# Performance work log

Hardware: AMD Instinct MI355X
Metric: run time of the kernel (lower is better)

The kernel has to match this reference:

```python
import jax, jax.numpy as jnp
import numpy as np
from jax import lax

B, D_MODEL, H, W = 8, 384, 64, 64
D_INNER, D_STATE, D_CONV, DT_RANK = 768, 16, 4, 24
C3, MLP_H = 3 * D_MODEL, 4 * D_MODEL
EPS = 1e-5


def setup_inputs():
    key = jax.random.key(0)
    ks = jax.random.split(key, 16)
    r = lambda i, shape, s=0.02: jax.random.normal(ks[i], shape, jnp.float32) * s
    return {
        'x': jax.random.normal(ks[0], (B, D_MODEL, H, W), jnp.float32),
        'ln1_g': jnp.ones((D_MODEL,), jnp.float32), 'ln1_b': jnp.zeros((D_MODEL,), jnp.float32),
        'in_w': r(1, (2 * D_INNER, D_MODEL)),
        'conv_w': r(2, (D_INNER, 1, D_CONV), 0.2), 'conv_b': jnp.zeros((D_INNER,), jnp.float32),
        'xproj_w': r(3, (DT_RANK + 2 * D_STATE, D_INNER)),
        'dtproj_w': r(4, (D_INNER, DT_RANK), 0.1),
        'dtproj_b': jnp.full((D_INNER,), jnp.log(jnp.expm1(0.01)).item(), jnp.float32),
        'A_log': jnp.log(jnp.broadcast_to(jnp.arange(1, D_STATE + 1, dtype=jnp.float32), (D_INNER, D_STATE))),
        'Dskip': jnp.ones((D_INNER,), jnp.float32),
        'out_w': r(5, (D_MODEL, D_INNER)),
        'dw_w': r(6, (C3, 1, 3, 3), 0.1),
        'bn_g': jnp.ones((C3,), jnp.float32), 'bn_b': jnp.zeros((C3,), jnp.float32),
        'bn_mean': jnp.zeros((C3,), jnp.float32), 'bn_var': jnp.ones((C3,), jnp.float32),
        'pw_w': r(7, (C3, C3)),
        'fus_w': r(8, (D_MODEL, D_MODEL)), 'fus_b': jnp.zeros((D_MODEL,), jnp.float32),
        'ln2_g': jnp.ones((D_MODEL,), jnp.float32), 'ln2_b': jnp.zeros((D_MODEL,), jnp.float32),
        'mlp_w1': r(9, (MLP_H, D_MODEL)), 'mlp_b1': jnp.zeros((MLP_H,), jnp.float32),
        'mlp_w2': r(10, (D_MODEL, MLP_H)), 'mlp_b2': jnp.zeros((D_MODEL,), jnp.float32),
    }


def _ln(x, g, b):
    m = x.mean(-1, keepdims=True)
    v = ((x - m) ** 2).mean(-1, keepdims=True)
    return (x - m) / jnp.sqrt(v + EPS) * g + b


def _dwt(x):
    x01 = x[:, :, 0::2, :] / 2
    x02 = x[:, :, 1::2, :] / 2
    x1, x3 = x01[:, :, :, 0::2], x01[:, :, :, 1::2]
    x2, x4 = x02[:, :, :, 0::2], x02[:, :, :, 1::2]
    ll = x1 + x2 + x3 + x4
    hl = -x1 - x2 + x3 + x4
    lh = -x1 + x2 - x3 + x4
    hh = x1 - x2 - x3 + x4
    return ll, jnp.concatenate([hl, lh, hh], axis=1)


def _idwt(ll, high):
    b, c, h, w = ll.shape
    hl, lh, hh = jnp.split(high, 3, axis=1)
    h_ll, h_hl, h_lh, h_hh = ll / 2, hl / 2, lh / 2, hh / 2
    y1 = h_ll - h_hl - h_lh + h_hh  # (even row, even col)
    y2 = h_ll - h_hl + h_lh - h_hh  # (odd row, even col)
    y3 = h_ll + h_hl - h_lh - h_hh  # (even row, odd col)
    y4 = h_ll + h_hl + h_lh + h_hh  # (odd row, odd col)
    row_e = jnp.stack([y1, y3], axis=-1).reshape(b, c, h, 2 * w)
    row_o = jnp.stack([y2, y4], axis=-1).reshape(b, c, h, 2 * w)
    return jnp.stack([row_e, row_o], axis=-2).reshape(b, c, 2 * h, 2 * w)


def _mamba(x, in_w, conv_w, conv_b, xproj_w, dtproj_w, dtproj_b, A_log, Dskip, out_w):
    # x: [B, L, d_model]
    bb = x.shape[0]
    xz = x @ in_w.T  # [B,L,2*d_inner]
    xi, z = jnp.split(xz, 2, axis=-1)
    xc = jnp.swapaxes(xi, 1, 2)  # [B,d_inner,L]
    xc = lax.conv_general_dilated(xc, conv_w, (1,), [(D_CONV - 1, 0)],
                                  feature_group_count=D_INNER,
                                  dimension_numbers=('NCH', 'OIH', 'NCH')) + conv_b[None, :, None]
    u = jax.nn.silu(jnp.swapaxes(xc, 1, 2))  # [B,L,d_inner]
    dbl = u @ xproj_w.T
    dtr = dbl[..., :DT_RANK]
    Bm = dbl[..., DT_RANK:DT_RANK + D_STATE]
    Cm = dbl[..., DT_RANK + D_STATE:]
    dt = jax.nn.softplus(dtr @ dtproj_w.T + dtproj_b)  # [B,L,d_inner]
    A = -jnp.exp(A_log)  # [d_inner,d_state]

    def step(h, t):
        dt_t, B_t, C_t, u_t = t
        dA = jnp.exp(dt_t[:, :, None] * A)
        h = dA * h + (dt_t * u_t)[:, :, None] * B_t[:, None, :]
        return h, jnp.sum(h * C_t[:, None, :], axis=-1)

    h0 = jnp.zeros((bb, D_INNER, D_STATE), x.dtype)
    xs = (jnp.swapaxes(dt, 0, 1), jnp.swapaxes(Bm, 0, 1), jnp.swapaxes(Cm, 0, 1), jnp.swapaxes(u, 0, 1))
    _, ys = lax.scan(step, h0, xs)
    y = jnp.swapaxes(ys, 0, 1) + u * Dskip
    y = y * jax.nn.silu(z)
    return y @ out_w.T


def reference(x, ln1_g, ln1_b, in_w, conv_w, conv_b, xproj_w, dtproj_w, dtproj_b,
              A_log, Dskip, out_w, dw_w, bn_g, bn_b, bn_mean, bn_var, pw_w,
              fus_w, fus_b, ln2_g, ln2_b, mlp_w1, mlp_b1, mlp_w2, mlp_b2):
    shortcut = x
    x_ll, x_high = _dwt(x)
    b, c, hh, ww = x_ll.shape
    # LL branch: LN -> Mamba -> residual
    x_ll_in = _ln(jnp.transpose(x_ll, (0, 2, 3, 1)), ln1_g, ln1_b)
    y = _mamba(x_ll_in.reshape(b, hh * ww, c), in_w, conv_w, conv_b, xproj_w,
               dtproj_w, dtproj_b, A_log, Dskip, out_w)
    x_ll_out = x_ll + jnp.transpose(y.reshape(b, hh, ww, c), (0, 3, 1, 2))
    # High-freq branch: depthwise3x3 -> BN(eval) -> SiLU -> 1x1 -> residual
    hd = lax.conv_general_dilated(x_high, dw_w, (1, 1), [(1, 1), (1, 1)],
                                  feature_group_count=C3,
                                  dimension_numbers=('NCHW', 'OIHW', 'NCHW'))
    hd = (hd - bn_mean[None, :, None, None]) / jnp.sqrt(bn_var + EPS)[None, :, None, None] \
         * bn_g[None, :, None, None] + bn_b[None, :, None, None]
    hd = jax.nn.silu(hd)
    x_high_out = x_high + jnp.einsum('bchw,oc->bohw', hd, pw_w)
    # Reconstruct + fusion 1x1 conv + residual
    recon = _idwt(x_ll_out, x_high_out)
    recon = jnp.einsum('bchw,oc->bohw', recon, fus_w) + fus_b[None, :, None, None]
    x2 = shortcut + recon
    # LN + MLP + residual
    xn = _ln(jnp.transpose(x2, (0, 2, 3, 1)), ln2_g, ln2_b)
    m = jax.nn.gelu(xn @ mlp_w1.T + mlp_b1, approximate=False) @ mlp_w2.T + mlp_b2
    return x2 + jnp.transpose(m, (0, 3, 1, 2))
```

## Files before the change

### kernel.cpp

```cpp
#include <hip/hip_runtime.h>
#include <hip/hip_bf16.h>
#include <math.h>

typedef __hip_bfloat16 bf16;
typedef __attribute__((ext_vector_type(8))) short bf16x8;
typedef __attribute__((ext_vector_type(4))) float f32x4;
typedef unsigned short u16;

#define LN_EPS 1e-5f

__device__ inline u16 f2b(float v) {
    __hip_bfloat16 h = __float2bfloat16(v);
    return *reinterpret_cast<u16*>(&h);
}

__device__ inline float b2f_lo(unsigned int w) { return __uint_as_float(w << 16); }
__device__ inline float b2f_hi(unsigned int w) { return __uint_as_float(w & 0xFFFF0000u); }

__device__ inline void gload_lds16(const void* g, void* l) {
    __builtin_amdgcn_global_load_lds(
        (const __attribute__((address_space(1))) void*)(uintptr_t)g,
        (__attribute__((address_space(3))) void*)(uintptr_t)(unsigned int)(uintptr_t)l,
        16, 0, 0);
}
__device__ inline void gload_lds4(const void* g, void* l) {
    __builtin_amdgcn_global_load_lds(
        (const __attribute__((address_space(1))) void*)(uintptr_t)g,
        (__attribute__((address_space(3))) void*)(uintptr_t)(unsigned int)(uintptr_t)l,
        4, 0, 0);
}

__global__ __launch_bounds__(256) void sentinel_kernel(float* __restrict__ out, int n) {
    int i = blockIdx.x * 256 + threadIdx.x;
    if (i < n) out[i] = 123.0f;
}

__global__ __launch_bounds__(256) void reduce12_kernel(const float* __restrict__ P,
                                                       float* __restrict__ out, int n4) {
    int i = blockIdx.x * 256 + threadIdx.x;
    if (i >= n4) return;
    const float4* p4 = (const float4*)P;
    float4 s = p4[i];
#pragma unroll
    for (int z = 1; z < 12; z++) {
        float4 v = p4[(size_t)z * n4 + i];
        s.x += v.x; s.y += v.y; s.z += v.z; s.w += v.w;
    }
    ((float4*)out)[i] = s;
}

__global__ void detect_kernel(const unsigned int* __restrict__ g, int* __restrict__ flag) {
    *flag = (*g == 0x3F803F80u) ? 1 : 0;
}

struct Jobs {
    const void* src[25];
    int prefix[26];
};
__global__ __launch_bounds__(256) void convert_kernel(Jobs J, u16* __restrict__ dst16,
                                                      float* __restrict__ dst32,
                                                      const int* __restrict__ flag) {
    int i = blockIdx.x * 256 + threadIdx.x;
    int total = J.prefix[25];
    if (i >= total) return;
    int f = *flag;
    int lo = 0;
    while (J.prefix[lo + 1] <= i) lo++;
    int off = i - J.prefix[lo];
    float v = f ? (float)((const bf16*)J.src[lo])[off] : ((const float*)J.src[lo])[off];
    if (lo < 6) dst16[i] = f2b(v);
    else        dst32[i - J.prefix[6]] = v;
}

__global__ __launch_bounds__(256) void dwt_kernel(const void* __restrict__ xv,
                                                  float* __restrict__ xll,
                                                  float* __restrict__ xhigh,
                                                  const int* __restrict__ flag) {
    __shared__ float tile[32][133];
    int blk = blockIdx.x;
    int cc = blk % 12;
    int t2 = blk / 12;
    int i  = t2 % 32;
    int b  = t2 / 32;
    int t  = threadIdx.x;
    int c_l = t >> 3;
    int sub = t & 7;
    size_t rowbase = ((size_t)(b * 384 + cc * 32 + c_l)) * 4096 + (size_t)i * 128;
    if (*flag) {
        const u16* xp = (const u16*)xv + rowbase;
#pragma unroll
        for (int k = 0; k < 2; k++) {
            int e0 = (sub + k * 8) * 8;
            uint4 v = *(const uint4*)(xp + e0);
            tile[c_l][e0 + 0] = b2f_lo(v.x); tile[c_l][e0 + 1] = b2f_hi(v.x);
            tile[c_l][e0 + 2] = b2f_lo(v.y); tile[c_l][e0 + 3] = b2f_hi(v.y);
            tile[c_l][e0 + 4] = b2f_lo(v.z); tile[c_l][e0 + 5] = b2f_hi(v.z);
            tile[c_l][e0 + 6] = b2f_lo(v.w); tile[c_l][e0 + 7] = b2f_hi(v.w);
        }
    } else {
        const float* xp = (const float*)xv + rowbase;
#pragma unroll
        for (int k = 0; k < 4; k++) {
            int f0 = (sub + k * 8) * 4;
            float4 v = *(const float4*)(xp + f0);
            tile[c_l][f0 + 0] = v.x; tile[c_l][f0 + 1] = v.y;
            tile[c_l][f0 + 2] = v.z; tile[c_l][f0 + 3] = v.w;
        }
    }
    __syncthreads();
    int c_out = t & 31;
    int jg = t >> 5;
    int cg = cc * 32 + c_out;
#pragma unroll
    for (int jj = 0; jj < 4; jj++) {
        int j = jg * 4 + jj;
        float A = tile[c_out][2 * j];
        float B = tile[c_out][2 * j + 1];
        float C = tile[c_out][64 + 2 * j];
        float D = tile[c_out][64 + 2 * j + 1];
        float ll = 0.5f * (A + B + C + D);
        float hl = 0.5f * (B + D - A - C);
        float lh = 0.5f * (C + D - A - B);
        float hh = 0.5f * (A + D - B - C);
        int pm = b * 1024 + i * 32 + j;
        xll[(size_t)pm * 384 + cg] = ll;
        size_t hb = (size_t)pm * 1152;
        xhigh[hb + cg] = hl;
        xhigh[hb + 384 + cg] = lh;
        xhigh[hb + 768 + cg] = hh;
    }
}

template <bool OBF>
__global__ __launch_bounds__(128) void ln_kernel(const float* __restrict__ in,
                                                 void* __restrict__ outv,
                                                 const float* __restrict__ g,
                                                 const float* __restrict__ b) {
    const int C = 384;
    int row = blockIdx.x;
    int t = threadIdx.x;
    const float* rp = in + (size_t)row * C;
    float v0 = rp[t], v1 = rp[t + 128], v2 = rp[t + 256];
    __shared__ float red[128];
    red[t] = v0 + v1 + v2;
    __syncthreads();
    for (int off = 64; off > 0; off >>= 1) {
        if (t < off) red[t] += red[t + off];
        __syncthreads();
    }
    float mean = red[0] * (1.f / 384.f);
    __syncthreads();
    float d0 = v0 - mean, d1 = v1 - mean, d2 = v2 - mean;
    red[t] = d0 * d0 + d1 * d1 + d2 * d2;
    __syncthreads();
    for (int off = 64; off > 0; off >>= 1) {
        if (t < off) red[t] += red[t + off];
        __syncthreads();
    }
    float inv = rsqrtf(red[0] * (1.f / 384.f) + LN_EPS);
    float o0 = d0 * inv * g[t]       + b[t];
    float o1 = d1 * inv * g[t + 128] + b[t + 128];
    float o2 = d2 * inv * g[t + 256] + b[t + 256];
    if constexpr (OBF) {
        u16* op = (u16*)outv + (size_t)row * C;
        op[t] = f2b(o0); op[t + 128] = f2b(o1); op[t + 256] = f2b(o2);
    } else {
        float* op = (float*)outv + (size_t)row * C;
        op[t] = o0; op[t + 128] = o1; op[t + 256] = o2;
    }
}

#define EP_NONE 0
#define EP_SOFTPLUS_BIAS 1
#define EP_ADD 2
#define EP_FUS 3
#define EP_GELU_BIAS 4
#define EP_FINAL 5

template <int EPIL, bool CBF>
__global__ __launch_bounds__(256) void gemm_mfma(const u16* __restrict__ A, int lda,
                                                 const u16* __restrict__ W,
                                                 void* __restrict__ Cp, int ldc,
                                                 int M, int N, int K,
                                                 const float* __restrict__ addsrc,
                                                 const float* __restrict__ bias,
                                                 const void* __restrict__ xres,
                                                 void* __restrict__ obf,
                                                 int m_off,
                                                 const int* __restrict__ flag) {
    __shared__ u16 Als[2][128][32];
    __shared__ u16 Bls[2][128][32];
    const int t = threadIdx.x;
    const int wave = t >> 6, lane = t & 63;
    const int quad = lane >> 4, r16 = lane & 15;
    const int wm = (wave >> 1) * 64, wn = (wave & 1) * 64;
    const int mb = blockIdx.x * 128, nb = blockIdx.y * 128;
    f32x4 acc[4][4] = {};

    const int srow = wave * 32 + (lane >> 2);
    const int scol = (lane & 3) * 8;
    const u16* Ag0 = A + (size_t)(mb + srow) * lda + scol;
    const u16* Ag1 = A + (size_t)(mb + srow + 16) * lda + scol;
    const u16* Wg0 = W + (size_t)(nb + srow) * (size_t)K + scol;
    const u16* Wg1 = W + (size_t)(nb + srow + 16) * (size_t)K + scol;

    gload_lds16(Ag0, &Als[0][wave * 32][0]);
    gload_lds16(Ag1, &Als[0][wave * 32 + 16][0]);
    gload_lds16(Wg0, &Bls[0][wave * 32][0]);
    gload_lds16(Wg1, &Bls[0][wave * 32 + 16][0]);
    __syncthreads();

    int cur = 0;
    for (int k0 = 0; k0 < K; k0 += 32) {
        int nxt = cur ^ 1;
        if (k0 + 32 < K) {
            gload_lds16(Ag0 + k0 + 32, &Als[nxt][wave * 32][0]);
            gload_lds16(Ag1 + k0 + 32, &Als[nxt][wave * 32 + 16][0]);
            gload_lds16(Wg0 + k0 + 32, &Bls[nxt][wave * 32][0]);
            gload_lds16(Wg1 + k0 + 32, &Bls[nxt][wave * 32 + 16][0]);
        }
        bf16x8 af[4], bfv[4];
#pragma unroll
        for (int i = 0; i < 4; i++) af[i] = *(const bf16x8*)&Als[cur][wm + i * 16 + r16][quad * 8];
#pragma unroll
        for (int j = 0; j < 4; j++) bfv[j] = *(const bf16x8*)&Bls[cur][wn + j * 16 + r16][quad * 8];
#pragma unroll
        for (int i = 0; i < 4; i++)
#pragma unroll
            for (int j = 0; j < 4; j++)
                acc[i][j] = __builtin_amdgcn_mfma_f32_16x16x32_bf16(af[i], bfv[j], acc[i][j], 0, 0, 0);
        __syncthreads();
        cur = nxt;
    }

    int f = 0;
    if constexpr (EPIL == EP_FUS || EPIL == EP_FINAL) f = *flag;
#pragma unroll
    for (int i = 0; i < 4; i++) {
#pragma unroll
        for (int j = 0; j < 4; j++) {
#pragma unroll
            for (int rg = 0; rg < 4; rg++) {
                int m = mb + wm + i * 16 + quad * 4 + rg;
                int n = nb + wn + j * 16 + r16;
                float v = acc[i][j][rg];
                if constexpr (EPIL == EP_NONE) {
                    if constexpr (CBF) ((u16*)Cp)[(size_t)m * ldc + n] = f2b(v);
                    else               ((float*)Cp)[(size_t)m * ldc + n] = v;
                } else if constexpr (EPIL == EP_ADD) {
                    ((float*)Cp)[(size_t)m * ldc + n] = addsrc[(size_t)m * ldc + n] + v;
                } else if constexpr (EPIL == EP_FUS) {
                    v += bias[n];
                    int bb = m >> 12, pix = m & 4095;
                    size_t xi = ((size_t)(bb * 384 + n) << 12) + pix;
                    v += f ? (float)((const bf16*)xres)[xi] : ((const float*)xres)[xi];
                    ((float*)Cp)[(size_t)m * ldc + n] = v;
                } else if constexpr (EPIL == EP_GELU_BIAS) {
                    v += bias[n];
                    v = 0.5f * v * (1.f + erff(v * 0.70710678118654752f));
                    if constexpr (CBF) ((u16*)Cp)[(size_t)m * ldc + n] = f2b(v);
                    else               ((float*)Cp)[(size_t)m * ldc + n] = v;
                } else if constexpr (EPIL == EP_FINAL) {
                    v += bias[n];
                    int gm = m_off + m;
                    v += addsrc[(size_t)gm * 384 + n];
                    int bb = gm >> 12, pix = gm & 4095;
                    size_t oi = ((size_t)(bb * 384 + n) << 12) + pix;
                    if (f) ((bf16*)obf)[oi] = __float2bfloat16(v);
                    else   ((float*)obf)[oi] = v;
                }
            }
        }
    }
}

template <int EPIL, bool SPLITK>
__global__ __launch_bounds__(256) void gemm_nt(const float* __restrict__ A, int lda,
                                               const float* __restrict__ W,
                                               float* __restrict__ C, int ldc,
                                               int M, int N, int K,
                                               const float* __restrict__ bias,
                                               int kc) {
    __shared__ __align__(16) float As[16][68];
    __shared__ __align__(16) float Bs[16][68];
    int t = threadIdx.x;
    int mb = blockIdx.y * 64;
    int nb = blockIdx.x * 64;
    int kb = SPLITK ? blockIdx.z * kc : 0;
    int ke = SPLITK ? kb + kc : K;
    int tm = t & 15, tn = t >> 4;
    float* Cout = C;
    if constexpr (SPLITK) Cout = C + (size_t)blockIdx.z * (size_t)M * ldc;
    float acc[4][4] = {};
    for (int k0 = kb; k0 < ke; k0 += 16) {
#pragma unroll
        for (int i = 0; i < 4; i++) {
            int idx = t + i * 256;
            int r = idx >> 4, c = idx & 15;
            float v = 0.f;
            if (k0 + c < K) v = A[(size_t)(mb + r) * lda + k0 + c];
            As[c][r] = v;
        }
#pragma unroll
        for (int i = 0; i < 4; i++) {
            int idx = t + i * 256;
            int r = idx >> 4, c = idx & 15;
            float v = 0.f;
            if ((nb + r) < N && (k0 + c) < K) v = W[(size_t)(nb + r) * K + k0 + c];
            Bs[c][r] = v;
        }
        __syncthreads();
#pragma unroll
        for (int kk = 0; kk < 16; kk++) {
            float4 av = *(const float4*)&As[kk][tm * 4];
            float4 bv = *(const float4*)&Bs[kk][tn * 4];
            float a4[4] = {av.x, av.y, av.z, av.w};
            float b4[4] = {bv.x, bv.y, bv.z, bv.w};
#pragma unroll
            for (int i = 0; i < 4; i++)
#pragma unroll
                for (int j = 0; j < 4; j++) acc[i][j] += a4[i] * b4[j];
        }
        __syncthreads();
    }
#pragma unroll
    for (int i = 0; i < 4; i++) {
        int m = mb + tm * 4 + i;
        if (m >= M) continue;
#pragma unroll
        for (int j = 0; j < 4; j++) {
            int n = nb + tn * 4 + j;
            if (n >= N) continue;
            float v = acc[i][j];
            if constexpr (SPLITK) {
                Cout[(size_t)m * ldc + n] = v;
            } else if constexpr (EPIL == EP_NONE) {
                C[(size_t)m * ldc + n] = v;
            } else if constexpr (EPIL == EP_SOFTPLUS_BIAS) {
                v += bias[n];
                v = (v > 20.f) ? v : log1pf(expf(v));
                C[(size_t)m * ldc + n] = v;
            }
        }
    }
}

__global__ __launch_bounds__(256) void conv1d_silu_kernel(const float* __restrict__ xz,
                                                          const float* __restrict__ cw,
                                                          const float* __restrict__ cb,
                                                          float* __restrict__ u) {
    int tid = blockIdx.x * 256 + threadIdx.x;
    int dq = tid % 192;
    int t2 = tid / 192;
    int l = t2 % 1024;
    int b = t2 / 1024;
    int d = dq * 4;
    float4 q0 = *(const float4*)&cw[d * 4];
    float4 q1 = *(const float4*)&cw[d * 4 + 4];
    float4 q2 = *(const float4*)&cw[d * 4 + 8];
    float4 q3 = *(const float4*)&cw[d * 4 + 12];
    float4 acc = *(const float4*)&cb[d];
    int rowbase = b * 1024;
#pragma unroll
    for (int k = 0; k < 4; k++) {
        int ls = l - 3 + k;
        if (ls < 0) continue;
        float4 xv = *(const float4*)&xz[(size_t)(rowbase + ls) * 1536 + d];
        acc.x += ((const float*)&q0)[k] * xv.x;
        acc.y += ((const float*)&q1)[k] * xv.y;
        acc.z += ((const float*)&q2)[k] * xv.z;
        acc.w += ((const float*)&q3)[k] * xv.w;
    }
    float4 o;
    o.x = acc.x / (1.f + __expf(-acc.x));
    o.y = acc.y / (1.f + __expf(-acc.y));
    o.z = acc.z / (1.f + __expf(-acc.z));
    o.w = acc.w / (1.f + __expf(-acc.w));
    *(float4*)&u[(size_t)(rowbase + l) * 768 + d] = o;
}

__device__ inline void scan_load_ac(const float* __restrict__ A_log, int d,
                                    float (&Ac)[16], bool& structured) {
#pragma unroll
    for (int s = 0; s < 16; s++) Ac[s] = -__expf(A_log[d * 16 + s]);
    structured = true;
#pragma unroll
    for (int s = 0; s < 16; s++)
        structured = structured && (fabsf(Ac[s] - (s + 1) * Ac[0]) <= 1e-5f * fabsf(Ac[s]));
}

__global__ __launch_bounds__(256) void scan_p1(const float* __restrict__ dt,
                                               const float* __restrict__ u,
                                               const float* __restrict__ dbl,
                                               const float* __restrict__ A_log,
                                               float* __restrict__ st) {
    __shared__ float Bsh[2][16][16];
    int tloc = threadIdx.x;
    int idx = blockIdx.x * 256 + tloc;
    int p = idx >> 1;
    int sh = idx & 1;
    int g = p % 6144;
    int c = p / 6144;
    int d = g % 768, b = g / 768;
    float Ac[16]; bool structured;
    scan_load_ac(A_log, d, Ac, structured);
    int s0 = sh * 8;
    float h[8];
#pragma unroll
    for (int s = 0; s < 8; s++) h[s] = 0.f;
    float S = 0.f;
    size_t m0 = (size_t)b * 1024 + c * 128;
    const int jj = tloc >> 4, ff = tloc & 15;
    float* lbase0 = &Bsh[0][0][0] + (tloc >> 6) * 64;
    float* lbase1 = &Bsh[1][0][0] + (tloc >> 6) * 64;
    gload_lds4(&dbl[(m0 + jj) * 56 + 24 + ff], lbase0);
    __syncthreads();
    for (int grp = 0; grp < 8; grp++) {
        int cur = grp & 1;
        if (grp + 1 < 8) {
            gload_lds4(&dbl[(m0 + (grp + 1) * 16 + jj) * 56 + 24 + ff],
                       cur ? lbase0 : lbase1);
        }
        float dtb[16], ub[16];
#pragma unroll
        for (int j = 0; j < 16; j++) {
            size_t m = m0 + grp * 16 + j;
            dtb[j] = dt[m * 768 + d];
            ub[j]  = u[m * 768 + d];
        }
        if (structured) {
#pragma unroll
            for (int j = 0; j < 16; j++) {
                float dtv = dtb[j];
                float du = dtv * ub[j];
                S += dtv;
                float q  = __expf(dtv * Ac[0]);
                float q2 = q * q, q3 = q2 * q, q4 = q2 * q2;
                float q5 = q4 * q, q6 = q4 * q2, q7 = q4 * q3, q8 = q4 * q4;
                float base = sh ? q8 : 1.f;
                float a[8] = {base * q,  base * q2, base * q3, base * q4,
                              base * q5, base * q6, base * q7, base * q8};
#pragma unroll
                for (int s = 0; s < 8; s++)
                    h[s] = a[s] * h[s] + du * Bsh[cur][j][s0 + s];
            }
        } else {
#pragma unroll
            for (int j = 0; j < 16; j++) {
                float dtv = dtb[j];
                float du = dtv * ub[j];
                S += dtv;
#pragma unroll
                for (int s = 0; s < 8; s++)
                    h[s] = __expf(dtv * Ac[s0 + s]) * h[s] + du * Bsh[cur][j][s0 + s];
            }
        }
        __syncthreads();
    }
    float* stp = st + (size_t)(c * 6144 + g) * 32;
#pragma unroll
    for (int s = 0; s < 8; s++) stp[s0 + s] = __expf(Ac[s0 + s] * S);
#pragma unroll
    for (int s = 0; s < 8; s++) stp[16 + s0 + s] = h[s];
}

__global__ __launch_bounds__(256) void scan_p2(float* __restrict__ st) {
    int tid = blockIdx.x * 256 + threadIdx.x;
    int s = tid & 15;
    int g = tid >> 4;
    float H = 0.f;
#pragma unroll
    for (int c = 0; c < 8; c++) {
        size_t i = (size_t)(c * 6144 + g) * 32;
        float P  = st[i + s];
        float hE = st[i + 16 + s];
        st[i + s] = H;
        H = hE + P * H;
    }
}

__global__ __launch_bounds__(256) void scan_p3(const float* __restrict__ dt,
                                               const float* __restrict__ u,
                                               const float* __restrict__ dbl,
                                               const float* __restrict__ z,
                                               const float* __restrict__ A_log,
                                               const float* __restrict__ Dskip,
                                               const float* __restrict__ st,
                                               u16* __restrict__ ybuf) {
    __shared__ float BCsh[2][8][32];
    int tloc = threadIdx.x;
    int idx = blockIdx.x * 256 + tloc;
    int p = idx >> 1;
    int sh = idx & 1;
    int g = p % 6144;
    int c = p / 6144;
    int d = g % 768, b = g / 768;
    float Ac[16]; bool structured;
    scan_load_ac(A_log, d, Ac, structured);
    int s0 = sh * 8;
    float Dsk = Dskip[d];
    float h[8];
    const float* stp = st + (size_t)(c * 6144 + g) * 32;
#pragma unroll
    for (int s = 0; s < 8; s++) h[s] = stp[s0 + s];
    size_t m0 = (size_t)b * 1024 + c * 128;
    const int jj = tloc >> 5, ff = tloc & 31;
    float* lbase0 = &BCsh[0][0][0] + (tloc >> 6) * 64;
    float* lbase1 = &BCsh[1][0][0] + (tloc >> 6) * 64;
    gload_lds4(&dbl[(m0 + jj) * 56 + 24 + ff], lbase0);
    __syncthreads();
    for (int grp = 0; grp < 16; grp++) {
        int cur = grp & 1;
        if (grp + 1 < 16) {
            gload_lds4(&dbl[(m0 + (grp + 1) * 8 + jj) * 56 + 24 + ff],
                       cur ? lbase0 : lbase1);
        }
        float dtb[8], ub[8], zb[8];
#pragma unroll
        for (int j = 0; j < 8; j++) {
            size_t m = m0 + grp * 8 + j;
            dtb[j] = dt[m * 768 + d];
            ub[j]  = u[m * 768 + d];
            zb[j]  = z[m * 1536 + 768 + d];
        }
#pragma unroll
        for (int j = 0; j < 8; j++) {
            size_t m = m0 + grp * 8 + j;
            float dtv = dtb[j];
            float uv  = ub[j];
            float zv  = zb[j];
            float du = dtv * uv;
            if (structured) {
                float q  = __expf(dtv * Ac[0]);
                float q2 = q * q, q3 = q2 * q, q4 = q2 * q2;
                float q5 = q4 * q, q6 = q4 * q2, q7 = q4 * q3, q8 = q4 * q4;
                float base = sh ? q8 : 1.f;
                float a[8] = {base * q,  base * q2, base * q3, base * q4,
                              base * q5, base * q6, base * q7, base * q8};
#pragma unroll
                for (int s = 0; s < 8; s++)
                    h[s] = a[s] * h[s] + du * BCsh[cur][j][s0 + s];
            } else {
#pragma unroll
                for (int s = 0; s < 8; s++)
                    h[s] = __expf(dtv * Ac[s0 + s]) * h[s] + du * BCsh[cur][j][s0 + s];
            }
            float pr[8];
#pragma unroll
            for (int s = 0; s < 8; s++) pr[s] = h[s] * BCsh[cur][j][16 + s0 + s];
            float y = ((pr[0] + pr[1]) + (pr[2] + pr[3])) + ((pr[4] + pr[5]) + (pr[6] + pr[7]));
            y += __shfl_xor(y, 1);
            if (!sh) {
                float sig = 1.f / (1.f + __expf(-zv));
                ybuf[m * 3072 + d] = f2b((y + uv * Dsk) * (zv * sig));
            }
        }
        __syncthreads();
    }
}

__global__ __launch_bounds__(256) void dwconv_bn_silu_kernel(const float* __restrict__ xh,
                                                             const float* __restrict__ w,
                                                             const float* __restrict__ g,
                                                             const float* __restrict__ bb,
                                                             const float* __restrict__ mean,
                                                             const float* __restrict__ var,
                                                             u16* __restrict__ hd) {
    int tid = blockIdx.x * 256 + threadIdx.x;
    int cq = tid % 288;
    int t2 = tid / 288;
    int xc = t2 & 3;
    int t3 = t2 >> 2;
    int y = t3 % 32;
    int b = t3 / 32;
    int c = cq * 4;
    float wk[9][4];
#pragma unroll
    for (int i = 0; i < 4; i++) {
        float4 wa = *(const float4*)&w[(c + i) * 9];
        float4 wbv = *(const float4*)&w[(c + i) * 9 + 4];
        float wcv = w[(c + i) * 9 + 8];
        wk[0][i] = wa.x; wk[1][i] = wa.y; wk[2][i] = wa.z; wk[3][i] = wa.w;
        wk[4][i] = wbv.x; wk[5][i] = wbv.y; wk[6][i] = wbv.z; wk[7][i] = wbv.w;
        wk[8][i] = wcv;
    }
    float4 mn = *(const float4*)&mean[c];
    float4 vr = *(const float4*)&var[c];
    float4 gg = *(const float4*)&g[c];
    float4 bv = *(const float4*)&bb[c];
    float scl[4], sft[4];
    scl[0] = rsqrtf(vr.x + LN_EPS) * gg.x; sft[0] = bv.x - mn.x * scl[0];
    scl[1] = rsqrtf(vr.y + LN_EPS) * gg.y; sft[1] = bv.y - mn.y * scl[1];
    scl[2] = rsqrtf(vr.z + LN_EPS) * gg.z; sft[2] = bv.z - mn.z * scl[2];
    scl[3] = rsqrtf(vr.w + LN_EPS) * gg.w; sft[3] = bv.w - mn.w * scl[3];

    int x0 = xc * 8;
    size_t pixbase = (size_t)b * 1024 + y * 32;
    float win[3][3][4];
    auto ldcol = [&](int xx, float (&col)[3][4]) {
#pragma unroll
        for (int r = 0; r < 3; r++) {
            int yy = y + r - 1;
            if (xx < 0 || xx > 31 || yy < 0 || yy > 31) {
                col[r][0] = col[r][1] = col[r][2] = col[r][3] = 0.f;
            } else {
                float4 v = *(const float4*)&xh[((size_t)b * 1024 + yy * 32 + xx) * 1152 + c];
                col[r][0] = v.x; col[r][1] = v.y; col[r][2] = v.z; col[r][3] = v.w;
            }
        }
    };
    ldcol(x0 - 1, win[0]);
    ldcol(x0, win[1]);
#pragma unroll
    for (int xi = 0; xi < 8; xi++) {
        int x = x0 + xi;
        ldcol(x + 1, win[2]);
        ushort4 o;
        u16* op = (u16*)&o;
#pragma unroll
        for (int i = 0; i < 4; i++) {
            float acc = 0.f;
#pragma unroll
            for (int ky = 0; ky < 3; ky++)
#pragma unroll
                for (int kx = 0; kx < 3; kx++)
                    acc += wk[ky * 3 + kx][i] * win[kx][ky][i];
            float vv = acc * scl[i] + sft[i];
            op[i] = f2b(vv / (1.f + __expf(-vv)));
        }
        *(ushort4*)&hd[(pixbase + x) * 1152 + c] = o;
#pragma unroll
        for (int r = 0; r < 3; r++)
#pragma unroll
            for (int i = 0; i < 4; i++) {
                win[0][r][i] = win[1][r][i];
                win[1][r][i] = win[2][r][i];
            }
    }
}

__global__ __launch_bounds__(256) void idwt_kernel(const float* __restrict__ xll,
                                                   const float* __restrict__ xh,
                                                   u16* __restrict__ recon) {
    int idx = blockIdx.x * 256 + threadIdx.x;
    int c = idx % 384;
    int t = idx / 384;
    int p = t % 1024;
    int b = t / 1024;
    int i = p >> 5, j = p & 31;
    float ll = xll[(size_t)(b * 1024 + p) * 384 + c];
    int hb = (b * 1024 + p) * 1152;
    float hl = xh[hb + c];
    float lh = xh[hb + 384 + c];
    float hh = xh[hb + 768 + c];
    float y1 = 0.5f * (ll - hl - lh + hh);
    float y3 = 0.5f * (ll + hl - lh - hh);
    float y2 = 0.5f * (ll - hl + lh - hh);
    float y4 = 0.5f * (ll + hl + lh + hh);
    int r0 = b * 4096 + (2 * i) * 64 + 2 * j;
    recon[(size_t)r0 * 384 + c] = f2b(y1);
    recon[(size_t)(r0 + 1) * 384 + c] = f2b(y3);
    recon[(size_t)(r0 + 64) * 384 + c] = f2b(y2);
    recon[(size_t)(r0 + 65) * 384 + c] = f2b(y4);
}

extern "C" void kernel_launch(void* const* d_in, const int* in_sizes, int n_in,
                              void* d_out, int out_size, void* d_ws, size_t ws_size,
                              hipStream_t stream) {
    const void* x = d_in[0];
    void* out = d_out;

    float* ws = (float*)d_ws;
    float* x_ll    = ws;
    float* x_high  = ws + 3145728;
    u16*   mlp_hid = (u16*)ws;
    float* xz      = ws + 12582912;
    u16*   ybuf    = (u16*)xz;
    u16*   hd      = (u16*)xz;
    u16*   recon   = (u16*)(ws + 17301504);
    u16*   xn      = recon;
    float* u       = ws + 25165824;
    float* dt      = ws + 31457280;
    u16*   x_ll_in = (u16*)dt;
    float* xpart   = dt;
    float* x2      = ws + 25165824;
    float* dbl     = ws + 37748736;
    float* scanst  = ws + 38207488;

    u16* wb16 = (u16*)(ws + 39780352);
    u16* b_in_w   = wb16;
    u16* b_out_w  = wb16 + 589824;
    u16* b_pw_w   = wb16 + 884736;
    u16* b_fus_w  = wb16 + 2211840;
    u16* b_mlp_w1 = wb16 + 2359296;
    u16* b_mlp_w2 = wb16 + 2949120;
    float* f32base = ws + 39780352 + 1769472;
    float* c_conv_w   = f32base;
    float* c_conv_b   = f32base + 3072;
    float* c_xproj_w  = f32base + 3840;
    float* c_dtproj_w = f32base + 46848;
    float* c_dtproj_b = f32base + 65280;
    float* c_A_log    = f32base + 66048;
    float* c_Dskip    = f32base + 78336;
    float* c_dw_w     = f32base + 79104;
    float* c_bn_g     = f32base + 89472;
    float* c_bn_b     = f32base + 90624;
    float* c_bn_mean  = f32base + 91776;
    float* c_bn_var   = f32base + 92928;
    float* c_ln1_g    = f32base + 94080;
    float* c_ln1_b    = f32base + 94464;
    float* c_ln2_g    = f32base + 94848;
    float* c_ln2_b    = f32base + 95232;
    float* c_fus_b    = f32base + 95616;
    float* c_mlp_b1   = f32base + 96000;
    float* c_mlp_b2   = f32base + 97536;
    int* flag = (int*)(f32base + 97920);

    if (ws_size < (size_t)(39780352 + 1769472 + 97920 + 2) * 4) {
        sentinel_kernel<<<(out_size + 255) / 256, 256, 0, stream>>>((float*)out, out_size);
        return;
    }

    detect_kernel<<<1, 1, 0, stream>>>((const unsigned int*)d_in[1], flag);
    Jobs J;
    const int src_idx[25] = {3, 11, 17, 18, 22, 24,
                             4, 5, 6, 7, 8, 9, 10, 12, 13, 14, 15, 16,
                             1, 2, 20, 21, 19, 23, 25};
    const int joff[26] = {0, 589824, 884736, 2211840, 2359296, 2949120, 3538944,
                          3538944 + 3072, 3538944 + 3840, 3538944 + 46848, 3538944 + 65280,
                          3538944 + 66048, 3538944 + 78336, 3538944 + 79104, 3538944 + 89472,
                          3538944 + 90624, 3538944 + 91776, 3538944 + 92928, 3538944 + 94080,
                          3538944 + 94464, 3538944 + 94848, 3538944 + 95232, 3538944 + 95616,
                          3538944 + 96000, 3538944 + 97536, 3538944 + 97920};
    for (int i = 0; i < 25; i++) J.src[i] = d_in[src_idx[i]];
    for (int i = 0; i < 26; i++) J.prefix[i] = joff[i];
    convert_kernel<<<(3636864 + 255) / 256, 256, 0, stream>>>(J, wb16, f32base, flag);

    dwt_kernel<<<3072, 256, 0, stream>>>(x, x_ll, x_high, flag);
    ln_kernel<true><<<8192, 128, 0, stream>>>(x_ll, x_ll_in, c_ln1_g, c_ln1_b);
    gemm_mfma<EP_NONE, false><<<dim3(64, 12), 256, 0, stream>>>(x_ll_in, 384, b_in_w, xz, 1536,
                                                                8192, 1536, 384, nullptr, nullptr, nullptr, nullptr, 0, flag);
    conv1d_silu_kernel<<<6144, 256, 0, stream>>>(xz, c_conv_w, c_conv_b, u);
    gemm_nt<EP_NONE, true><<<dim3(1, 128, 12), 256, 0, stream>>>(u, 768, c_xproj_w, xpart, 56,
                                                                 8192, 56, 768, nullptr, 64);
    reduce12_kernel<<<(114688 + 255) / 256, 256, 0, stream>>>(xpart, dbl, 114688);
    gemm_nt<EP_SOFTPLUS_BIAS, false><<<dim3(12, 128), 256, 0, stream>>>(dbl, 56, c_dtproj_w, dt, 768,
                                                                        8192, 768, 24, c_dtproj_b, 0);
    scan_p1<<<384, 256, 0, stream>>>(dt, u, dbl, c_A_log, scanst);
    scan_p2<<<384, 256, 0, stream>>>(scanst);
    scan_p3<<<384, 256, 0, stream>>>(dt, u, dbl, xz, c_A_log, c_Dskip, scanst, ybuf);
    gemm_mfma<EP_ADD, false><<<dim3(64, 3), 256, 0, stream>>>(ybuf, 3072, b_out_w, x_ll, 384,
                                                              8192, 384, 768, x_ll, nullptr, nullptr, nullptr, 0, flag);
    dwconv_bn_silu_kernel<<<1152, 256, 0, stream>>>(x_high, c_dw_w, c_bn_g, c_bn_b, c_bn_mean, c_bn_var, hd);
    gemm_mfma<EP_ADD, false><<<dim3(64, 9), 256, 0, stream>>>(hd, 1152, b_pw_w, x_high, 1152,
                                                              8192, 1152, 1152, x_high, nullptr, nullptr, nullptr, 0, flag);
    idwt_kernel<<<12288, 256, 0, stream>>>(x_ll, x_high, recon);
    gemm_mfma<EP_FUS, false><<<dim3(256, 3), 256, 0, stream>>>(recon, 384, b_fus_w, x2, 384,
                                                               32768, 384, 384, nullptr, c_fus_b, x, nullptr, 0, flag);
    ln_kernel<true><<<32768, 128, 0, stream>>>(x2, xn, c_ln2_g, c_ln2_b);
    for (int ck = 0; ck < 2; ck++) {
        const u16* xn_c = xn + (size_t)ck * 16384 * 384;
        gemm_mfma<EP_GELU_BIAS, true><<<dim3(128, 12), 256, 0, stream>>>(xn_c, 384, b_mlp_w1, mlp_hid, 1536,
                                                                         16384, 1536, 384, nullptr, c_mlp_b1, nullptr, nullptr, 0, flag);
        gemm_mfma<EP_FINAL, false><<<dim3(128, 3), 256, 0, stream>>>(mlp_hid, 1536, b_mlp_w2, nullptr, 0,
                                                                     16384, 384, 1536, x2, c_mlp_b2, nullptr, out, ck * 16384, flag);
    }
}
```

Baseline: 711.8 us.

## Triple-buffer GEMM LDS tiles with explicit vmcnt waits and one barrier

The MFMA GEMM moves from a double-buffered LDS pipeline to a triple-buffered one. It prefetches two K-tiles ahead and uses explicit s_waitcnt vmcnt counts plus a single barrier per iteration, replacing the trailing __syncthreads. The goal is to hide more global-to-LDS load latency and remove one barrier per K step. The cost is 50% more LDS per block, which may reduce occupancy. Correctness depends on the vmcnt accounting matching the four loads per stage.

Measured after the change: 692.8 us. 1.03x faster.

```diff
diff --git a/kernel.cpp b/kernel.cpp
--- a/kernel.cpp
+++ b/kernel.cpp
@@ -188,8 +188,8 @@
                                                  void* __restrict__ obf,
                                                  int m_off,
                                                  const int* __restrict__ flag) {
-    __shared__ u16 Als[2][128][32];
-    __shared__ u16 Bls[2][128][32];
+    __shared__ u16 Als[3][128][32];
+    __shared__ u16 Bls[3][128][32];
     const int t = threadIdx.x;
     const int wave = t >> 6, lane = t & 63;
     const int quad = lane >> 4, r16 = lane & 15;
@@ -204,33 +204,36 @@
     const u16* Wg0 = W + (size_t)(nb + srow) * (size_t)K + scol;
     const u16* Wg1 = W + (size_t)(nb + srow + 16) * (size_t)K + scol;
 
-    gload_lds16(Ag0, &Als[0][wave * 32][0]);
-    gload_lds16(Ag1, &Als[0][wave * 32 + 16][0]);
-    gload_lds16(Wg0, &Bls[0][wave * 32][0]);
-    gload_lds16(Wg1, &Bls[0][wave * 32 + 16][0]);
-    __syncthreads();
-
-    int cur = 0;
-    for (int k0 = 0; k0 < K; k0 += 32) {
-        int nxt = cur ^ 1;
-        if (k0 + 32 < K) {
-            gload_lds16(Ag0 + k0 + 32, &Als[nxt][wave * 32][0]);
-            gload_lds16(Ag1 + k0 + 32, &Als[nxt][wave * 32 + 16][0]);
-            gload_lds16(Wg0 + k0 + 32, &Bls[nxt][wave * 32][0]);
-            gload_lds16(Wg1 + k0 + 32, &Bls[nxt][wave * 32 + 16][0]);
-        }
+    auto stage = [&](int buf, int kt) {
+        int k0 = kt * 32;
+        gload_lds16(Ag0 + k0, &Als[buf][wave * 32][0]);
+        gload_lds16(Ag1 + k0, &Als[buf][wave * 32 + 16][0]);
+        gload_lds16(Wg0 + k0, &Bls[buf][wave * 32][0]);
+        gload_lds16(Wg1 + k0, &Bls[buf][wave * 32 + 16][0]);
+    };
+
+    const int NK = K >> 5;
+    stage(0, 0);
+    if (NK > 1) stage(1, 1);
+
+    for (int kt = 0; kt < NK; kt++) {
+        if (kt + 1 < NK) asm volatile("s_waitcnt vmcnt(4)" ::: "memory");
+        else             asm volatile("s_waitcnt vmcnt(0)" ::: "memory");
+        __builtin_amdgcn_s_barrier();
+        asm volatile("" ::: "memory");
+        int pf = kt + 2;
+        if (pf < NK) stage(pf % 3, pf);
+        const int cb = kt % 3;
         bf16x8 af[4], bfv[4];
 #pragma unroll
-        for (int i = 0; i < 4; i++) af[i] = *(const bf16x8*)&Als[cur][wm + i * 16 + r16][quad * 8];
-#pragma unroll
-        for (int j = 0; j < 4; j++) bfv[j] = *(const bf16x8*)&Bls[cur][wn + j * 16 + r16][quad * 8];
+        for (int i = 0; i < 4; i++) af[i] = *(const bf16x8*)&Als[cb][wm + i * 16 + r16][quad * 8];
+#pragma unroll
+        for (int j = 0; j < 4; j++) bfv[j] = *(const bf16x8*)&Bls[cb][wn + j * 16 + r16][quad * 8];
 #pragma unroll
         for (int i = 0; i < 4; i++)
 #pragma unroll
             for (int j = 0; j < 4; j++)
                 acc[i][j] = __builtin_amdgcn_mfma_f32_16x16x32_bf16(af[i], bfv[j], acc[i][j], 0, 0, 0);
-        __syncthreads();
-        cur = nxt;
     }
 
     int f = 0;
```
